# Kernel optimization log

Measured on AMD Instinct MI355X. Metric: run time of the kernel, lower is better.

## Reference

```python
import jax, jax.numpy as jnp
import numpy as np

N_NODES = 100000
N_EDGES = 600000
IN_FEATS = 128
N_HIDDEN = 128
N_CLASSES = 64


def _glorot(key, shape):
    fan_in, fan_out = shape[1], shape[0]
    lim = np.sqrt(6.0 / (fan_in + fan_out)).astype(np.float32)
    return jax.random.uniform(key, shape, jnp.float32, -lim, lim)


def setup_inputs() -> dict:
    key = jax.random.key(0)
    ks = jax.random.split(key, 12)
    x = jax.random.normal(ks[0], (N_NODES, IN_FEATS), jnp.float32)
    edge_src = jax.random.randint(ks[1], (N_EDGES,), 0, N_NODES, jnp.int64 if jax.config.jax_enable_x64 else jnp.int32)
    edge_dst = jax.random.randint(ks[2], (N_EDGES,), 0, N_NODES, jnp.int64 if jax.config.jax_enable_x64 else jnp.int32)
    dims = [(IN_FEATS, N_HIDDEN), (N_HIDDEN, N_HIDDEN), (N_HIDDEN, N_CLASSES)]
    inp = {"x": x, "edge_src": edge_src, "edge_dst": edge_dst}
    for i, (din, dout) in enumerate(dims, start=1):
        inp[f"W_self{i}"] = _glorot(ks[2 + 3 * i], (dout, din))
        inp[f"W_neigh{i}"] = _glorot(ks[3 + 3 * i], (dout, din))
        inp[f"b{i}"] = jnp.zeros((dout,), jnp.float32)
    return inp


def _sage_conv(h, edge_src, edge_dst, W_self, W_neigh, b):
    # mean-aggregate neighbor features: gather at src, segment-mean at dst
    msgs = h[edge_src]                                   # [E, din] irregular gather
    agg = jax.ops.segment_sum(msgs, edge_dst, num_segments=h.shape[0])
    deg = jax.ops.segment_sum(jnp.ones_like(edge_dst, dtype=h.dtype), edge_dst,
                              num_segments=h.shape[0])
    h_neigh = agg / jnp.maximum(deg, 1.0)[:, None]
    # fc_self(h) + fc_neigh(h_neigh) + bias  (DGL SAGEConv 'mean')
    return h @ W_self.T + h_neigh @ W_neigh.T + b


def reference(x, edge_src, edge_dst,
              W_self1, W_neigh1, b1,
              W_self2, W_neigh2, b2,
              W_self3, W_neigh3, b3):
    h = _sage_conv(x, edge_src, edge_dst, W_self1, W_neigh1, b1)
    h = jax.nn.relu(h)  # dropout is identity at inference
    h = _sage_conv(h, edge_src, edge_dst, W_self2, W_neigh2, b2)
    h = jax.nn.relu(h)
    h = _sage_conv(h, edge_src, edge_dst, W_self3, W_neigh3, b3)
    return h
```

## Files before the change

kernel.cpp:

```cpp
#include <hip/hip_runtime.h>

#define NN 100000
#define NE 600000
#define FD 128
#define NB ((NN + 255) / 256)

typedef __attribute__((ext_vector_type(8))) short bf16x8;
typedef __attribute__((ext_vector_type(4))) float f32x4;

__device__ __forceinline__ unsigned short f2bf(float x) {
    unsigned int u = __float_as_uint(x);
    u += 0x7FFFu + ((u >> 16) & 1u);
    return (unsigned short)(u >> 16);
}

__global__ __launch_bounds__(256) void hist_kernel(const int* __restrict__ dst,
                                                   int* __restrict__ cnt, int E) {
    int e = blockIdx.x * 256 + threadIdx.x;
    if (e < E) atomicAdd(&cnt[dst[e]], 1);
}

__global__ __launch_bounds__(256) void scan_blocks(const int* __restrict__ cnt,
                                                   int* __restrict__ bsum) {
    __shared__ int s[256];
    int i = blockIdx.x * 256 + threadIdx.x;
    int t = threadIdx.x;
    s[t] = (i < NN) ? cnt[i] : 0;
    __syncthreads();
    for (int off = 128; off > 0; off >>= 1) {
        if (t < off) s[t] += s[t + off];
        __syncthreads();
    }
    if (t == 0) bsum[blockIdx.x] = s[0];
}

__global__ __launch_bounds__(512) void scan_top(int* __restrict__ bsum,
                                                int* __restrict__ row_ptr) {
    __shared__ int s[512];
    int t = threadIdx.x;
    int v = (t < NB) ? bsum[t] : 0;
    s[t] = v;
    __syncthreads();
    for (int off = 1; off < 512; off <<= 1) {
        int x = (t >= off) ? s[t - off] : 0;
        __syncthreads();
        s[t] += x;
        __syncthreads();
    }
    if (t < NB) bsum[t] = s[t] - v;
    if (t == 0) row_ptr[NN] = NE;
}

__global__ __launch_bounds__(256) void scan_write(const int* __restrict__ cnt,
                                                  const int* __restrict__ bofs,
                                                  int* __restrict__ row_ptr) {
    __shared__ int s[256];
    int i = blockIdx.x * 256 + threadIdx.x;
    int t = threadIdx.x;
    int v = (i < NN) ? cnt[i] : 0;
    s[t] = v;
    __syncthreads();
    for (int off = 1; off < 256; off <<= 1) {
        int x = (t >= off) ? s[t - off] : 0;
        __syncthreads();
        s[t] += x;
        __syncthreads();
    }
    if (i < NN) row_ptr[i] = s[t] - v + bofs[blockIdx.x];
}

__global__ __launch_bounds__(256) void fill_kernel(const int* __restrict__ src,
                                                   const int* __restrict__ dst,
                                                   int* __restrict__ cursor,
                                                   int* __restrict__ col, int E) {
    int e = blockIdx.x * 256 + threadIdx.x;
    if (e < E) {
        int p = atomicAdd(&cursor[dst[e]], 1);
        col[p] = src[e];
    }
}

__global__ __launch_bounds__(256) void cvt_kernel(const float* __restrict__ x,
                                                  unsigned short* __restrict__ xb,
                                                  int n4) {
    int i = blockIdx.x * 256 + threadIdx.x;
    if (i < n4) {
        float4 v = reinterpret_cast<const float4*>(x)[i];
        uint2 o;
        o.x = (unsigned)f2bf(v.x) | ((unsigned)f2bf(v.y) << 16);
        o.y = (unsigned)f2bf(v.z) | ((unsigned)f2bf(v.w) << 16);
        reinterpret_cast<uint2*>(xb)[i] = o;
    }
}

__global__ __launch_bounds__(256) void wcvt_kernel(const float* __restrict__ Ws,
                                                   const float* __restrict__ Wn,
                                                   unsigned short* __restrict__ Wb,
                                                   int rows) {
    int tid = blockIdx.x * 256 + threadIdx.x;
    if (tid >= rows * 64) return;
    int row = tid >> 6;
    int k   = (tid & 63) * 4;
    const float* src = (k < 128) ? (Ws + (size_t)row * 128 + k)
                                 : (Wn + (size_t)row * 128 + (k - 128));
    float4 v = *reinterpret_cast<const float4*>(src);
    uint2 o;
    o.x = (unsigned)f2bf(v.x) | ((unsigned)f2bf(v.y) << 16);
    o.y = (unsigned)f2bf(v.z) | ((unsigned)f2bf(v.w) << 16);
    *reinterpret_cast<uint2*>(Wb + (size_t)row * 256 + k) = o;
}

__device__ __forceinline__ void bf2_acc(unsigned v, float& ax, float& ay) {
    ax += __uint_as_float(v << 16);
    ay += __uint_as_float(v & 0xFFFF0000u);
}

__global__ __launch_bounds__(256) void agg_kernel(const unsigned short* __restrict__ h,
                                                  const int* __restrict__ rp,
                                                  const int* __restrict__ col,
                                                  unsigned short* __restrict__ agg) {
    int w    = (blockIdx.x * 256 + threadIdx.x) >> 6;
    int lane = threadIdx.x & 63;
    if (w >= NN) return;
    int beg = __builtin_amdgcn_readfirstlane(rp[w]);
    int end = __builtin_amdgcn_readfirstlane(rp[w + 1]);
    const unsigned short* hl = h + lane * 2;
    float ax = 0.f, ay = 0.f;
    int e = beg;
    for (; e + 4 <= end; e += 4) {
        int s0 = col[e + 0], s1 = col[e + 1], s2 = col[e + 2], s3 = col[e + 3];
        unsigned v0 = *reinterpret_cast<const unsigned*>(hl + (size_t)s0 * FD);
        unsigned v1 = *reinterpret_cast<const unsigned*>(hl + (size_t)s1 * FD);
        unsigned v2 = *reinterpret_cast<const unsigned*>(hl + (size_t)s2 * FD);
        unsigned v3 = *reinterpret_cast<const unsigned*>(hl + (size_t)s3 * FD);
        bf2_acc(v0, ax, ay);
        bf2_acc(v1, ax, ay);
        bf2_acc(v2, ax, ay);
        bf2_acc(v3, ax, ay);
    }
    if (e + 2 <= end) {
        int s0 = col[e + 0], s1 = col[e + 1];
        unsigned v0 = *reinterpret_cast<const unsigned*>(hl + (size_t)s0 * FD);
        unsigned v1 = *reinterpret_cast<const unsigned*>(hl + (size_t)s1 * FD);
        bf2_acc(v0, ax, ay);
        bf2_acc(v1, ax, ay);
        e += 2;
    }
    if (e < end) {
        int s0 = col[e];
        unsigned v0 = *reinterpret_cast<const unsigned*>(hl + (size_t)s0 * FD);
        bf2_acc(v0, ax, ay);
    }
    float inv = 1.0f / fmaxf((float)(end - beg), 1.0f);
    ax *= inv;
    ay *= inv;
    *reinterpret_cast<unsigned*>(agg + (size_t)w * FD + lane * 2) =
        (unsigned)f2bf(ax) | ((unsigned)f2bf(ay) << 16);
}

template <int NWC, bool RELU, bool OUTBF16, int OSTRIDE>
__global__ __launch_bounds__(256) void mfma_gemm(const unsigned short* __restrict__ Ah,
                                                 const unsigned short* __restrict__ Ag,
                                                 const unsigned short* __restrict__ Wb,
                                                 const float* __restrict__ bias,
                                                 void* __restrict__ outp) {
    constexpr int TR   = (4 / NWC) * 16;
    constexpr int NTIL = NN / TR;

    const int t   = threadIdx.x;
    const int w   = t >> 6;
    const int l   = t & 63;
    const int lo4 = l & 15;
    const int hi  = l >> 4;
    const int jw      = (w % NWC) * 32;
    const int row_off = (w / NWC) * 16;

    bf16x8 breg[2][8];
#pragma unroll
    for (int f = 0; f < 2; ++f)
#pragma unroll
        for (int ks = 0; ks < 8; ++ks)
            breg[f][ks] = *reinterpret_cast<const bf16x8*>(
                Wb + (size_t)(jw + f * 16 + lo4) * 256 + ks * 32 + hi * 8);

    unsigned short* hout = (unsigned short*)outp;
    float* fout = (float*)outp;
    const float bv0 = bias[jw + lo4];
    const float bv1 = bias[jw + 16 + lo4];

    for (int tile = blockIdx.x; tile < NTIL; tile += gridDim.x) {
        const int row = tile * TR + row_off + lo4;
        const unsigned short* Ar = Ah + (size_t)row * FD;
        const unsigned short* Gr = Ag + (size_t)row * FD;
        bf16x8 a[8];
#pragma unroll
        for (int ks = 0; ks < 4; ++ks)
            a[ks] = *reinterpret_cast<const bf16x8*>(Ar + ks * 32 + hi * 8);
#pragma unroll
        for (int ks = 0; ks < 4; ++ks)
            a[4 + ks] = *reinterpret_cast<const bf16x8*>(Gr + ks * 32 + hi * 8);

        f32x4 acc0 = {0.f, 0.f, 0.f, 0.f};
        f32x4 acc1 = {0.f, 0.f, 0.f, 0.f};
#pragma unroll
        for (int ks = 0; ks < 8; ++ks) {
            acc0 = __builtin_amdgcn_mfma_f32_16x16x32_bf16(a[ks], breg[0][ks], acc0, 0, 0, 0);
            acc1 = __builtin_amdgcn_mfma_f32_16x16x32_bf16(a[ks], breg[1][ks], acc1, 0, 0, 0);
        }

        const int rbase = tile * TR + row_off + hi * 4;
#pragma unroll
        for (int r = 0; r < 4; ++r) {
            float v0 = acc0[r] + bv0;
            float v1 = acc1[r] + bv1;
            if (RELU) { v0 = fmaxf(v0, 0.f); v1 = fmaxf(v1, 0.f); }
            const size_t n = (size_t)(rbase + r);
            if (OUTBF16) {
                hout[n * OSTRIDE + jw + lo4]      = f2bf(v0);
                hout[n * OSTRIDE + jw + 16 + lo4] = f2bf(v1);
            } else {
                fout[n * OSTRIDE + jw + lo4]      = v0;
                fout[n * OSTRIDE + jw + 16 + lo4] = v1;
            }
        }
    }
}

extern "C" void kernel_launch(void* const* d_in, const int* in_sizes, int n_in,
                              void* d_out, int out_size, void* d_ws, size_t ws_size,
                              hipStream_t stream) {
    const float* x        = (const float*)d_in[0];
    const int*   edge_src = (const int*)d_in[1];
    const int*   edge_dst = (const int*)d_in[2];
    const float* Ws1 = (const float*)d_in[3];
    const float* Wn1 = (const float*)d_in[4];
    const float* b1  = (const float*)d_in[5];
    const float* Ws2 = (const float*)d_in[6];
    const float* Wn2 = (const float*)d_in[7];
    const float* b2  = (const float*)d_in[8];
    const float* Ws3 = (const float*)d_in[9];
    const float* Wn3 = (const float*)d_in[10];
    const float* b3  = (const float*)d_in[11];
    float* out = (float*)d_out;

    unsigned short* x_bf = (unsigned short*)d_ws;
    unsigned short* h_a  = x_bf + (size_t)NN * FD;
    unsigned short* h_b  = h_a + (size_t)NN * FD;
    unsigned short* aggb = h_b + (size_t)NN * FD;
    int* cursor = (int*)(aggb + (size_t)NN * FD);
    int* bsum   = (int*)aggb;
    int* col_src = (int*)d_out;
    int* row_ptr = col_src + NE;
    unsigned short* wb1 = (unsigned short*)(col_src + NE + NN + 4);
    unsigned short* wb2 = wb1 + 128 * 256;
    unsigned short* wb3 = (unsigned short*)cursor;

    const int edgeGrid = (NE + 255) / 256;
    const int aggGrid  = NN / 4;

    cvt_kernel<<<(NN * FD / 4 + 255) / 256, 256, 0, stream>>>(x, x_bf, NN * FD / 4);
    wcvt_kernel<<<32, 256, 0, stream>>>(Ws1, Wn1, wb1, 128);
    wcvt_kernel<<<32, 256, 0, stream>>>(Ws2, Wn2, wb2, 128);

    hipMemsetAsync(cursor, 0, (size_t)NN * sizeof(int), stream);
    hist_kernel<<<edgeGrid, 256, 0, stream>>>(edge_dst, cursor, NE);
    scan_blocks<<<NB, 256, 0, stream>>>(cursor, bsum);
    scan_top<<<1, 512, 0, stream>>>(bsum, row_ptr);
    scan_write<<<NB, 256, 0, stream>>>(cursor, bsum, row_ptr);
    hipMemcpyAsync(cursor, row_ptr, (size_t)NN * sizeof(int),
                   hipMemcpyDeviceToDevice, stream);
    fill_kernel<<<edgeGrid, 256, 0, stream>>>(edge_src, edge_dst, cursor,
                                              col_src, NE);
    wcvt_kernel<<<16, 256, 0, stream>>>(Ws3, Wn3, wb3, 64);

    agg_kernel<<<aggGrid, 256, 0, stream>>>(x_bf, row_ptr, col_src, aggb);
    mfma_gemm<4, true, true, 128><<<1024, 256, 0, stream>>>(
        x_bf, aggb, wb1, b1, h_a);

    agg_kernel<<<aggGrid, 256, 0, stream>>>(h_a, row_ptr, col_src, aggb);
    mfma_gemm<4, true, true, 128><<<1024, 256, 0, stream>>>(
        h_a, aggb, wb2, b2, h_b);

    agg_kernel<<<aggGrid, 256, 0, stream>>>(h_b, row_ptr, col_src, aggb);
    mfma_gemm<2, false, false, 64><<<1024, 256, 0, stream>>>(
        h_b, aggb, wb3, b3, out);
}
```

Before: 366.0 us.

## Fuse prep conversions, unroll gather by eight, pack GEMM output stores

Merges the x and three weight conversion kernels into one prep launch, which cuts the launch count. The neighbor aggregation loop is rewritten as a fixed 8-wide unrolled gather with clamped indices and masking. This raises loads in flight but issues wasted loads when degree is low. The GEMM output columns are remapped so each lane writes two adjacent columns as one packed store, and the workspace layout is moved so nothing is staged in the output buffer.

```diff
diff --git a/kernel.cpp b/kernel.cpp
--- a/kernel.cpp
+++ b/kernel.cpp
@@ -80,25 +80,8 @@
     }
 }
 
-__global__ __launch_bounds__(256) void cvt_kernel(const float* __restrict__ x,
-                                                  unsigned short* __restrict__ xb,
-                                                  int n4) {
-    int i = blockIdx.x * 256 + threadIdx.x;
-    if (i < n4) {
-        float4 v = reinterpret_cast<const float4*>(x)[i];
-        uint2 o;
-        o.x = (unsigned)f2bf(v.x) | ((unsigned)f2bf(v.y) << 16);
-        o.y = (unsigned)f2bf(v.z) | ((unsigned)f2bf(v.w) << 16);
-        reinterpret_cast<uint2*>(xb)[i] = o;
-    }
-}
-
-__global__ __launch_bounds__(256) void wcvt_kernel(const float* __restrict__ Ws,
-                                                   const float* __restrict__ Wn,
-                                                   unsigned short* __restrict__ Wb,
-                                                   int rows) {
-    int tid = blockIdx.x * 256 + threadIdx.x;
-    if (tid >= rows * 64) return;
+__device__ __forceinline__ void wcvt_body(const float* Ws, const float* Wn,
+                                          unsigned short* Wb, int tid) {
     int row = tid >> 6;
     int k   = (tid & 63) * 4;
     const float* src = (k < 128) ? (Ws + (size_t)row * 128 + k)
@@ -110,9 +93,33 @@
     *reinterpret_cast<uint2*>(Wb + (size_t)row * 256 + k) = o;
 }
 
-__device__ __forceinline__ void bf2_acc(unsigned v, float& ax, float& ay) {
-    ax += __uint_as_float(v << 16);
-    ay += __uint_as_float(v & 0xFFFF0000u);
+__global__ __launch_bounds__(256) void prep_kernel(const float* __restrict__ x,
+                                                   unsigned short* __restrict__ xb,
+                                                   const float* __restrict__ Ws1,
+                                                   const float* __restrict__ Wn1,
+                                                   unsigned short* __restrict__ Wb1,
+                                                   const float* __restrict__ Ws2,
+                                                   const float* __restrict__ Wn2,
+                                                   unsigned short* __restrict__ Wb2,
+                                                   const float* __restrict__ Ws3,
+                                                   const float* __restrict__ Wn3,
+                                                   unsigned short* __restrict__ Wb3) {
+    int b = blockIdx.x;
+    int t = threadIdx.x;
+    if (b < 12500) {
+        int i = b * 256 + t;
+        float4 v = reinterpret_cast<const float4*>(x)[i];
+        uint2 o;
+        o.x = (unsigned)f2bf(v.x) | ((unsigned)f2bf(v.y) << 16);
+        o.y = (unsigned)f2bf(v.z) | ((unsigned)f2bf(v.w) << 16);
+        reinterpret_cast<uint2*>(xb)[i] = o;
+    } else if (b < 12532) {
+        wcvt_body(Ws1, Wn1, Wb1, (b - 12500) * 256 + t);
+    } else if (b < 12564) {
+        wcvt_body(Ws2, Wn2, Wb2, (b - 12532) * 256 + t);
+    } else {
+        wcvt_body(Ws3, Wn3, Wb3, (b - 12564) * 256 + t);
+    }
 }
 
 __global__ __launch_bounds__(256) void agg_kernel(const unsigned short* __restrict__ h,
@@ -126,30 +133,19 @@
     int end = __builtin_amdgcn_readfirstlane(rp[w + 1]);
     const unsigned short* hl = h + lane * 2;
     float ax = 0.f, ay = 0.f;
-    int e = beg;
-    for (; e + 4 <= end; e += 4) {
-        int s0 = col[e + 0], s1 = col[e + 1], s2 = col[e + 2], s3 = col[e + 3];
-        unsigned v0 = *reinterpret_cast<const unsigned*>(hl + (size_t)s0 * FD);
-        unsigned v1 = *reinterpret_cast<const unsigned*>(hl + (size_t)s1 * FD);
-        unsigned v2 = *reinterpret_cast<const unsigned*>(hl + (size_t)s2 * FD);
-        unsigned v3 = *reinterpret_cast<const unsigned*>(hl + (size_t)s3 * FD);
-        bf2_acc(v0, ax, ay);
-        bf2_acc(v1, ax, ay);
-        bf2_acc(v2, ax, ay);
-        bf2_acc(v3, ax, ay);
-    }
-    if (e + 2 <= end) {
-        int s0 = col[e + 0], s1 = col[e + 1];
-        unsigned v0 = *reinterpret_cast<const unsigned*>(hl + (size_t)s0 * FD);
-        unsigned v1 = *reinterpret_cast<const unsigned*>(hl + (size_t)s1 * FD);
-        bf2_acc(v0, ax, ay);
-        bf2_acc(v1, ax, ay);
-        e += 2;
-    }
-    if (e < end) {
-        int s0 = col[e];
-        unsigned v0 = *reinterpret_cast<const unsigned*>(hl + (size_t)s0 * FD);
-        bf2_acc(v0, ax, ay);
+    if (beg < end) {
+        int last = end - 1;
+        for (int e = beg; e < end; e += 8) {
+#pragma unroll
+            for (int i = 0; i < 8; ++i) {
+                int ee  = e + i;
+                int idx = col[ee <= last ? ee : last];
+                unsigned v = *reinterpret_cast<const unsigned*>(hl + (size_t)idx * FD);
+                if (ee > last) v = 0u;
+                ax += __uint_as_float(v << 16);
+                ay += __uint_as_float(v & 0xFFFF0000u);
+            }
+        }
     }
     float inv = 1.0f / fmaxf((float)(end - beg), 1.0f);
     ax *= inv;
@@ -181,12 +177,12 @@
 #pragma unroll
         for (int ks = 0; ks < 8; ++ks)
             breg[f][ks] = *reinterpret_cast<const bf16x8*>(
-                Wb + (size_t)(jw + f * 16 + lo4) * 256 + ks * 32 + hi * 8);
+                Wb + (size_t)(jw + 2 * lo4 + f) * 256 + ks * 32 + hi * 8);
 
     unsigned short* hout = (unsigned short*)outp;
     float* fout = (float*)outp;
-    const float bv0 = bias[jw + lo4];
-    const float bv1 = bias[jw + 16 + lo4];
+    const float bv0 = bias[jw + 2 * lo4];
+    const float bv1 = bias[jw + 2 * lo4 + 1];
 
     for (int tile = blockIdx.x; tile < NTIL; tile += gridDim.x) {
         const int row = tile * TR + row_off + lo4;
@@ -216,11 +212,11 @@
             if (RELU) { v0 = fmaxf(v0, 0.f); v1 = fmaxf(v1, 0.f); }
             const size_t n = (size_t)(rbase + r);
             if (OUTBF16) {
-                hout[n * OSTRIDE + jw + lo4]      = f2bf(v0);
-                hout[n * OSTRIDE + jw + 16 + lo4] = f2bf(v1);
+                unsigned pk = (unsigned)f2bf(v0) | ((unsigned)f2bf(v1) << 16);
+                *reinterpret_cast<unsigned*>(hout + n * OSTRIDE + jw + 2 * lo4) = pk;
             } else {
-                fout[n * OSTRIDE + jw + lo4]      = v0;
-                fout[n * OSTRIDE + jw + 16 + lo4] = v1;
+                *reinterpret_cast<float2*>(fout + n * OSTRIDE + jw + 2 * lo4) =
+                    make_float2(v0, v1);
             }
         }
     }
@@ -247,20 +243,19 @@
     unsigned short* h_a  = x_bf + (size_t)NN * FD;
     unsigned short* h_b  = h_a + (size_t)NN * FD;
     unsigned short* aggb = h_b + (size_t)NN * FD;
-    int* cursor = (int*)(aggb + (size_t)NN * FD);
-    int* bsum   = (int*)aggb;
-    int* col_src = (int*)d_out;
+    unsigned short* wb1  = aggb + (size_t)NN * FD;
+    unsigned short* wb2  = wb1 + 128 * 256;
+    unsigned short* wb3  = wb2 + 128 * 256;
+    int* cursor  = (int*)(wb3 + 64 * 256);
+    int* col_src = cursor + NN;
     int* row_ptr = col_src + NE;
-    unsigned short* wb1 = (unsigned short*)(col_src + NE + NN + 4);
-    unsigned short* wb2 = wb1 + 128 * 256;
-    unsigned short* wb3 = (unsigned short*)cursor;
+    int* bsum    = row_ptr + (NN + 1);
 
     const int edgeGrid = (NE + 255) / 256;
     const int aggGrid  = NN / 4;
 
-    cvt_kernel<<<(NN * FD / 4 + 255) / 256, 256, 0, stream>>>(x, x_bf, NN * FD / 4);
-    wcvt_kernel<<<32, 256, 0, stream>>>(Ws1, Wn1, wb1, 128);
-    wcvt_kernel<<<32, 256, 0, stream>>>(Ws2, Wn2, wb2, 128);
+    prep_kernel<<<12580, 256, 0, stream>>>(x, x_bf, Ws1, Wn1, wb1,
+                                           Ws2, Wn2, wb2, Ws3, Wn3, wb3);
 
     hipMemsetAsync(cursor, 0, (size_t)NN * sizeof(int), stream);
     hist_kernel<<<edgeGrid, 256, 0, stream>>>(edge_dst, cursor, NE);
@@ -271,7 +266,6 @@
                    hipMemcpyDeviceToDevice, stream);
     fill_kernel<<<edgeGrid, 256, 0, stream>>>(edge_src, edge_dst, cursor,
                                               col_src, NE);
-    wcvt_kernel<<<16, 256, 0, stream>>>(Ws3, Wn3, wb3, 64);
 
     agg_kernel<<<aggGrid, 256, 0, stream>>>(x_bf, row_ptr, col_src, aggb);
     mfma_gemm<4, true, true, 128><<<1024, 256, 0, stream>>>(
```

After: 363.9 us. Within noise of the previous version (-0.6%).
